# Optimization experiments

Hardware: AMD Instinct MI355X
Metric: run time of the kernel (lower is better)

The kernel has to match this reference:

```python
import jax, jax.numpy as jnp
import numpy as np

# Static configuration (matches init_kwargs)
EMBED_DIM = 256
NUM_HEADS = 8
NUM_LEVELS = 4
NUM_POINTS = 16
N_DEGREE = 3
HEAD_DIM = EMBED_DIM // NUM_HEADS
SPATIAL_SHAPES = ((64, 64), (32, 32), (16, 16), (8, 8))  # (H, W) per level
LEN_V = sum(h * w for h, w in SPATIAL_SHAPES)


def _bilinear_gather(v, loc, Hl, Wl):
    """Bilinear sampling with zero padding, align_corners=False.
    v:   [bs, nH, Hl*Wl, hd]  flattened level feature map (per head)
    loc: [bs, nH, Q, 2]       (x, y) in [0, 1]
    returns [bs, nH, Q, hd]
    """
    x = loc[..., 0] * Wl - 0.5
    y = loc[..., 1] * Hl - 0.5
    x0 = jnp.floor(x)
    y0 = jnp.floor(y)
    wx = x - x0
    wy = y - y0
    out = jnp.zeros(v.shape[:2] + (loc.shape[2], v.shape[-1]), v.dtype)
    corners = ((0, 0, (1 - wx) * (1 - wy)), (1, 0, wx * (1 - wy)),
               (0, 1, (1 - wx) * wy), (1, 1, wx * wy))
    for dx, dy, w in corners:
        xi = x0 + dx
        yi = y0 + dy
        valid = (xi >= 0) & (xi < Wl) & (yi >= 0) & (yi < Hl)
        idx = (jnp.clip(yi, 0, Hl - 1) * Wl + jnp.clip(xi, 0, Wl - 1)).astype(jnp.int32)
        g = jnp.take_along_axis(v, idx[..., None], axis=2)  # [bs,nH,Q,hd]
        out = out + g * (w * valid.astype(w.dtype))[..., None]
    return out


def setup_inputs() -> dict:
    key = jax.random.key(0)
    ks = jax.random.split(key, 12)
    bs, Lq = 4, 1024
    s = 0.02
    return {
        "query": jax.random.normal(ks[0], (bs, Lq, EMBED_DIM), jnp.float32),
        # polynomial coefficients for x(l), y(l); scaled so curves stay roughly in [0,1]
        "reference_points": jax.random.uniform(ks[1], (bs, Lq, 2 * (N_DEGREE + 1)), jnp.float32) * 0.25,
        "value": jax.random.normal(ks[2], (bs, LEN_V, EMBED_DIM), jnp.float32),
        "W_value": jax.random.normal(ks[3], (EMBED_DIM, EMBED_DIM), jnp.float32) * s,
        "b_value": jnp.zeros((EMBED_DIM,), jnp.float32),
        "W_offsets": jax.random.normal(ks[4], (EMBED_DIM, NUM_HEADS * NUM_LEVELS * NUM_POINTS * 2), jnp.float32) * s,
        "b_offsets": jax.random.normal(ks[5], (NUM_HEADS * NUM_LEVELS * NUM_POINTS * 2,), jnp.float32) * 0.5,
        "W_attn": jax.random.normal(ks[6], (EMBED_DIM, NUM_HEADS * NUM_LEVELS * NUM_POINTS), jnp.float32) * s,
        "b_attn": jnp.zeros((NUM_HEADS * NUM_LEVELS * NUM_POINTS,), jnp.float32),
        "W_out": jax.random.normal(ks[7], (EMBED_DIM, EMBED_DIM), jnp.float32) * s,
        "b_out": jnp.zeros((EMBED_DIM,), jnp.float32),
    }


def reference(query, reference_points, value, W_value, b_value, W_offsets,
              b_offsets, W_attn, b_attn, W_out, b_out):
    bs, Lq, _ = query.shape
    Lv = value.shape[1]
    nH, nL, nP, hd = NUM_HEADS, NUM_LEVELS, NUM_POINTS, HEAD_DIM

    v = (value @ W_value + b_value).reshape(bs, Lv, nH, hd)

    sampling_offsets = (query @ W_offsets + b_offsets).reshape(bs, Lq, nH, nL, nP, 2)
    attn = jax.nn.softmax((query @ W_attn + b_attn).reshape(bs, Lq, nH, nL * nP), axis=-1)
    attn = attn.reshape(bs, Lq, nH, nL, nP)

    # reference_points last dim == 8: polynomial branch
    lambdaz = jnp.linspace(0.0, 1.0, nP)
    lambdas = jnp.stack([lambdaz ** i for i in range(N_DEGREE, -1, -1)], axis=1)  # [nP, deg+1]
    ref_polys = reference_points.reshape(bs, Lq, 2, N_DEGREE + 1)
    pnts = jnp.einsum('bqcd,pd->bqpc', ref_polys, lambdas)  # [bs,Lq,nP,2] (x,y)

    # offset_normalizer: spatial shapes flipped -> (W, H) per level
    normalizer = jnp.array([[w, h] for (h, w) in SPATIAL_SHAPES], jnp.float32)
    normalizer = normalizer.reshape(1, 1, 1, nL, 1, 2)
    sampling_locations = pnts[:, :, None, None, :, :] + sampling_offsets / normalizer
    # -> [bs, Lq, nH, nL, nP, 2] in [0,1]

    # deformable attention core: per-level bilinear gather + softmax-weighted sum
    out = jnp.zeros((bs, Lq, nH, hd), v.dtype)
    start = 0
    for lvl, (Hl, Wl) in enumerate(SPATIAL_SHAPES):
        v_l = v[:, start:start + Hl * Wl].transpose(0, 2, 1, 3)  # [bs,nH,Hl*Wl,hd]
        loc_l = sampling_locations[:, :, :, lvl]                 # [bs,Lq,nH,nP,2]
        loc_l = loc_l.transpose(0, 2, 1, 3, 4).reshape(bs, nH, Lq * nP, 2)
        sampled = _bilinear_gather(v_l, loc_l, Hl, Wl).reshape(bs, nH, Lq, nP, hd)
        out = out + jnp.einsum('bhqpd,bqhp->bqhd', sampled, attn[:, :, :, lvl])
        start += Hl * Wl

    output = out.reshape(bs, Lq, nH * hd) @ W_out + b_out
    return output, sampling_locations, attn
```

## Files before the change

### kernel.cpp

```cpp
#include <hip/hip_runtime.h>
#include <math.h>

#define BS 4
#define LQ 1024
#define EMB 256
#define NH 8
#define NL 4
#define NP 16
#define HD 32
#define LV 5440
#define LVP 5936
#define KDIM 256

typedef __attribute__((ext_vector_type(8))) short short8;
typedef __attribute__((ext_vector_type(4))) float f32x4;

__device__ inline unsigned short f2bf(float f) {
    unsigned u = __builtin_bit_cast(unsigned, f);
    u += 0x7fff + ((u >> 16) & 1);
    return (unsigned short)(u >> 16);
}



__global__ __launch_bounds__(256) void prep(const float* __restrict__ Wv,
                                            const float* __restrict__ Wo,
                                            const float* __restrict__ Wa,
                                            const float* __restrict__ Wu,
                                            const float* __restrict__ value,
                                            const float* __restrict__ query,
                                            unsigned short* __restrict__ Wt,
                                            unsigned short* __restrict__ val_bf,
                                            unsigned short* __restrict__ qry_bf,
                                            unsigned short* __restrict__ v_pad) {
    const int blk = blockIdx.x;
    const int t = threadIdx.x;
    if (blk < 512) {
        __shared__ float tile[32][33];
        const int n0 = (blk & 63) * 32, k0 = (blk >> 6) * 32;
        const float* src; int N, nloc;
        if (n0 < 256)       { src = Wv; N = 256;  nloc = n0; }
        else if (n0 < 1280) { src = Wo; N = 1024; nloc = n0 - 256; }
        else if (n0 < 1792) { src = Wa; N = 512;  nloc = n0 - 1280; }
        else                { src = Wu; N = 256;  nloc = n0 - 1792; }
        const int tx = t & 31, ty = t >> 5;
#pragma unroll
        for (int i = 0; i < 32; i += 8)
            tile[ty + i][tx] = src[(size_t)(k0 + ty + i) * N + nloc + tx];
        __syncthreads();
        if (t < 128) {
            const int n_loc = t & 31, oct = t >> 5;
            const int n = n0 + n_loc;
            short8 h;
#pragma unroll
            for (int e = 0; e < 8; ++e) h[e] = (short)f2bf(tile[oct * 8 + e][n_loc]);
            const size_t off = ((size_t)(n >> 4) * 8 + (k0 >> 5)) * 512
                             + ((n & 15) + 16 * oct) * 8;
            *(short8*)(Wt + off) = h;
        }
    } else if (blk < 3744) {
        int i; const float* src; unsigned short* dst;
        if (blk < 3232) { i = (blk - 512) * 256 + t;  src = value; dst = val_bf; }
        else            { i = (blk - 3232) * 256 + t; src = query; dst = qry_bf; }
        const int r = i >> 5, oct = i & 31, k0 = oct * 8;
        const float4 f0 = *(const float4*)(src + (size_t)r * KDIM + k0);
        const float4 f1 = *(const float4*)(src + (size_t)r * KDIM + k0 + 4);
        short8 h;
        h[0] = (short)f2bf(f0.x); h[1] = (short)f2bf(f0.y);
        h[2] = (short)f2bf(f0.z); h[3] = (short)f2bf(f0.w);
        h[4] = (short)f2bf(f1.x); h[5] = (short)f2bf(f1.y);
        h[6] = (short)f2bf(f1.z); h[7] = (short)f2bf(f1.w);
        const size_t off = ((size_t)(r >> 4) * 8 + (oct >> 2)) * 512
                         + ((r & 15) + 16 * (oct & 3)) * 8;
        *(short8*)(dst + off) = h;
    } else {
        const int pidx = (blk - 3744) * 8 + (t >> 5);
        const int lane32 = t & 31;
        const unsigned b = (unsigned)pidx / 496u;
        const unsigned rem = (unsigned)pidx - b * 496u;
        int Wd, W2, pb, i;
        if (rem < 260)      { Wd = 64; W2 = 66; pb = 0;    i = rem; }
        else if (rem < 392) { Wd = 32; W2 = 34; pb = 4356; i = rem - 260; }
        else if (rem < 460) { Wd = 16; W2 = 18; pb = 5512; i = rem - 392; }
        else                { Wd = 8;  W2 = 10; pb = 5836; i = rem - 460; }
        int y, x;
        if (i < W2)          { y = 0;      x = i; }
        else if (i < 2 * W2) { y = Wd + 1; x = i - W2; }
        else { const int j = i - 2 * W2; y = 1 + (j >> 1); x = (j & 1) ? (Wd + 1) : 0; }
        const int hh = lane32 >> 2, cq = lane32 & 3;
        const size_t off = (((size_t)(hh * BS + b) * LVP + pb + y * W2 + x) << 5)
                         + cq * 8;
        uint4 z = {0, 0, 0, 0};
        *(uint4*)(v_pad + off) = z;
    }
}

template <int MODE>
__device__ __forceinline__ void gemm_nolds(const unsigned short* __restrict__ A,
                                           const unsigned short* __restrict__ Bt,
                                           const float* __restrict__ bias,
                                           const float* __restrict__ bias2,
                                           const float* __restrict__ refp,
                                           void* __restrict__ Cv,
                                           float* __restrict__ C2,
                                           int N, int bx, int by) {
    const int t = threadIdx.x;
    const int lane = t & 63, w = t >> 6;
    const int quad = lane >> 4, l16 = lane & 15;
    const int wr = w >> 1, wc = w & 1;
    const int row0 = by * 128, col0 = bx * 128;

    const unsigned short* ap = A  + ((size_t)((row0 >> 4) + wr * 4) * 8) * 512 + lane * 8;
    const unsigned short* bp = Bt + ((size_t)((col0 >> 4) + wc * 4) * 8) * 512 + lane * 8;

    f32x4 acc[4][4] = {};

#pragma unroll 2
    for (int kt = 0; kt < 8; ++kt) {
        short8 af[4], bf[4];
#pragma unroll
        for (int mi = 0; mi < 4; ++mi)
            af[mi] = *(const short8*)(ap + (size_t)mi * 4096 + kt * 512);
#pragma unroll
        for (int ni = 0; ni < 4; ++ni)
            bf[ni] = *(const short8*)(bp + (size_t)ni * 4096 + kt * 512);
#pragma unroll
        for (int mi = 0; mi < 4; ++mi)
#pragma unroll
            for (int ni = 0; ni < 4; ++ni)
                acc[mi][ni] = __builtin_amdgcn_mfma_f32_16x16x32_bf16(af[mi], bf[ni],
                                                                      acc[mi][ni], 0, 0, 0);
    }

    if (MODE == 0) {
#pragma unroll
        for (int ni = 0; ni < 4; ++ni) {
            const int c = col0 + wc * 64 + ni * 16 + l16;
            const float bv = bias[c];
#pragma unroll
            for (int mi = 0; mi < 4; ++mi) {
                const int r0 = row0 + wr * 64 + mi * 16 + quad * 4;
#pragma unroll
                for (int rr = 0; rr < 4; ++rr)
                    ((float*)Cv)[(size_t)(r0 + rr) * N + c] = acc[mi][ni][rr] + bv;
            }
        }
    } else if (MODE == 2) {
        unsigned short* C = (unsigned short*)Cv;
        float bv[4];
        int cc[4];
#pragma unroll
        for (int ni = 0; ni < 4; ++ni) {
            cc[ni] = col0 + wc * 64 + ni * 16 + l16;
            bv[ni] = bias[cc[ni]];
        }
#pragma unroll
        for (int mi = 0; mi < 4; ++mi) {
#pragma unroll
            for (int rr = 0; rr < 4; ++rr) {
                const unsigned r = row0 + wr * 64 + mi * 16 + quad * 4 + rr;
                const unsigned b = r / 5440u;
                const unsigned flat = r - b * 5440u;
                unsigned y, x, W2, pb;
                if (flat < 4096)      { y = flat >> 6; x = flat & 63; W2 = 66; pb = 0; }
                else if (flat < 5120) { const unsigned f = flat - 4096; y = f >> 5; x = f & 31; W2 = 34; pb = 4356; }
                else if (flat < 5376) { const unsigned f = flat - 5120; y = f >> 4; x = f & 15; W2 = 18; pb = 5512; }
                else                  { const unsigned f = flat - 5376; y = f >> 3; x = f & 7;  W2 = 10; pb = 5836; }
                const size_t pix = (size_t)(pb + (y + 1) * W2 + (x + 1)) << 5;
#pragma unroll
                for (int ni = 0; ni < 4; ++ni) {
                    const int cc_ = cc[ni];
                    const size_t off = (((size_t)((cc_ >> 5) * BS + b) * LVP) << 5)
                                     + pix + (cc_ & 31);
                    C[off] = f2bf(acc[mi][ni][rr] + bv[ni]);
                }
            }
        }
    } else {
        const bool is_off = (col0 < 1024);
        if (is_off) {
            float* C = (float*)Cv;
#pragma unroll
            for (int ni = 0; ni < 4; ++ni) {
                const int cg = col0 + wc * 64 + ni * 16 + l16;
                const int xy = cg & 1, p = (cg >> 1) & 15, l = (cg >> 5) & 3;
                const float lam = (float)p * (1.0f / 15.0f);
                const float l2 = lam * lam, l3 = l2 * lam;
                const float rW = (l == 0) ? 0.015625f : (l == 1) ? 0.03125f
                                : (l == 2) ? 0.0625f : 0.125f;
                const float bv = bias[cg];
#pragma unroll
                for (int mi = 0; mi < 4; ++mi) {
                    const int r0 = row0 + wr * 64 + mi * 16 + quad * 4;
#pragma unroll
                    for (int rr = 0; rr < 4; ++rr) {
                        const int r = r0 + rr;
                        const float4 rp = *(const float4*)(refp + (size_t)r * 8 + xy * 4);
                        const float poly = rp.x * l3 + rp.y * l2 + rp.z * lam + rp.w;
                        C[(size_t)r * 1024 + cg] = poly + (acc[mi][ni][rr] + bv) * rW;
                    }
                }
            }
        } else {
            const int cabase = col0 - 1024 + wc * 64;
            float bv[4];
#pragma unroll
            for (int ni = 0; ni < 4; ++ni) bv[ni] = bias2[cabase + ni * 16 + l16];
#pragma unroll
            for (int mi = 0; mi < 4; ++mi) {
                const int r0 = row0 + wr * 64 + mi * 16 + quad * 4;
#pragma unroll
                for (int rr = 0; rr < 4; ++rr) {
                    float v0 = acc[mi][0][rr] + bv[0];
                    float v1 = acc[mi][1][rr] + bv[1];
                    float v2 = acc[mi][2][rr] + bv[2];
                    float v3 = acc[mi][3][rr] + bv[3];
                    float mx = fmaxf(fmaxf(v0, v1), fmaxf(v2, v3));
#pragma unroll
                    for (int mk = 1; mk < 16; mk <<= 1) mx = fmaxf(mx, __shfl_xor(mx, mk));
                    v0 = __expf(v0 - mx); v1 = __expf(v1 - mx);
                    v2 = __expf(v2 - mx); v3 = __expf(v3 - mx);
                    float s = v0 + v1 + v2 + v3;
#pragma unroll
                    for (int mk = 1; mk < 16; mk <<= 1) s += __shfl_xor(s, mk);
                    const float inv = 1.0f / s;
                    const size_t rb = (size_t)(r0 + rr) * 512 + cabase + l16;
                    C2[rb]      = v0 * inv;
                    C2[rb + 16] = v1 * inv;
                    C2[rb + 32] = v2 * inv;
                    C2[rb + 48] = v3 * inv;
                }
            }
        }
    }
}

__global__ __launch_bounds__(256, 2) void gemm_fused(const unsigned short* __restrict__ val_bf,
                                                     const unsigned short* __restrict__ qry_bf,
                                                     const unsigned short* __restrict__ Wt,
                                                     const float* __restrict__ b_value,
                                                     const float* __restrict__ b_off,
                                                     const float* __restrict__ b_attn,
                                                     const float* __restrict__ refp,
                                                     unsigned short* __restrict__ v_pad,
                                                     float* __restrict__ loc_out,
                                                     float* __restrict__ attn_out) {
    const int b = blockIdx.x;
    if (b < 340) {
        gemm_nolds<2>(val_bf, Wt, b_value, nullptr, nullptr,
                      v_pad, nullptr, 256, b & 1, b >> 1);
    } else {
        const int b2 = b - 340;
        gemm_nolds<1>(qry_bf, Wt + (size_t)256 * KDIM, b_off, b_attn, refp,
                      loc_out, attn_out, 1536, b2 % 12, b2 / 12);
    }
}

__global__ __launch_bounds__(256, 2) void gemm_outp(const unsigned short* __restrict__ interm,
                                                    const unsigned short* __restrict__ Wt_out,
                                                    const float* __restrict__ b_out,
                                                    float* __restrict__ out) {
    gemm_nolds<0>(interm, Wt_out, b_out, nullptr, nullptr,
                  out, nullptr, 256, blockIdx.x & 1, blockIdx.x >> 1);
}

__global__ __launch_bounds__(256, 8) void sample_kernel(const unsigned short* __restrict__ v,
                                                        const float* __restrict__ loc,
                                                        const float* __restrict__ attn,
                                                        unsigned short* __restrict__ interm) {
    const int t = threadIdx.x;
    const int h = blockIdx.x & 7;
    const int bq0 = (blockIdx.x >> 3) * 16;

    __shared__ float4 wls[1088];
    __shared__ unsigned short pls[1088];

    {
        const int gloc = t >> 4;
        const int lvl  = (t >> 2) & 3;
        const int pq   = t & 3;
        const int g = (bq0 + gloc) * 8 + h;
        const float4 l01 = *(const float4*)(loc + (size_t)g * 128 + lvl * 32 + pq * 8);
        const float4 l23 = *(const float4*)(loc + (size_t)g * 128 + lvl * 32 + pq * 8 + 4);
        const float4 av  = *(const float4*)(attn + (size_t)g * 64 + lvl * 16 + pq * 4);
        const int Wd = 64 >> lvl;
        const float Wf = (float)Wd;
        const int W2 = Wd + 2;
        const int pb = (lvl == 0) ? 0 : (lvl == 1) ? 4356 : (lvl == 2) ? 5512 : 5836;
        const int ibase = gloc * 64 + lvl * 16 + pq * 4;
        const int pbase = ibase + (ibase >> 4);
        const float lx[4] = {l01.x, l01.z, l23.x, l23.z};
        const float ly[4] = {l01.y, l01.w, l23.y, l23.w};
        const float aw[4] = {av.x, av.y, av.z, av.w};
#pragma unroll
        for (int k = 0; k < 4; ++k) {
            const float x = fmaf(lx[k], Wf, -0.5f);
            const float y = fmaf(ly[k], Wf, -0.5f);
            const float xc = fminf(fmaxf(x, -1.0f), Wf);
            const float yc = fminf(fmaxf(y, -1.0f), Wf);
            const float x0f = fminf(floorf(xc), Wf - 1.0f);
            const float y0f = fminf(floorf(yc), Wf - 1.0f);
            const float wx = xc - x0f, wy = yc - y0f;
            const float iwx = 1.0f - wx, iwy = 1.0f - wy;
            const int px = (int)x0f + 1;
            const int py = (int)y0f + 1;
            const float a = aw[k];
            wls[pbase + k] = make_float4(iwx * iwy * a, wx * iwy * a,
                                         iwx * wy * a,  wx * wy * a);
            pls[pbase + k] = (unsigned short)(pb + py * W2 + px);
        }
    }
    __syncthreads();

    const int bq = bq0 + (t >> 4);
    const int l16i = t & 15;
    const int lvl = l16i >> 2;
    const int cq  = l16i & 3;
    const int b = bq >> 10;
    const int rowoff = ((64 >> lvl) + 2) * 32;

    const unsigned short* vl = v + (((size_t)(h * BS + b) * LVP) << 5) + cq * 8;
    const int wbase = (t >> 4) * 64 + lvl * 16;
    const int wphys = wbase + (wbase >> 4);

    float2 acc2[4] = {};

    auto cvt2 = [](unsigned d) {
        uint2 u; u.x = d << 16; u.y = d & 0xffff0000u;
        return __builtin_bit_cast(float2, u);
    };
    auto cadd = [&](const uint4 q, float wgt) {
        const float2 w2 = make_float2(wgt, wgt);
        acc2[0] += cvt2(q.x) * w2;
        acc2[1] += cvt2(q.y) * w2;
        acc2[2] += cvt2(q.z) * w2;
        acc2[3] += cvt2(q.w) * w2;
    };

#pragma unroll 1
    for (int p = 0; p < 16; ++p) {
        const float4 w = wls[wphys + p];
        const int base = ((int)pls[wphys + p]) << 5;
        const unsigned short* ptr = vl + base;
        const uint4 g00 = *(const uint4*)(ptr);
        const uint4 g10 = *(const uint4*)(ptr + 32);
        const uint4 g01 = *(const uint4*)(ptr + rowoff);
        const uint4 g11 = *(const uint4*)(ptr + rowoff + 32);
        cadd(g00, w.x); cadd(g10, w.y); cadd(g01, w.z); cadd(g11, w.w);
    }

    float a[8] = {acc2[0].x, acc2[0].y, acc2[1].x, acc2[1].y,
                  acc2[2].x, acc2[2].y, acc2[3].x, acc2[3].y};
#pragma unroll
    for (int m = 4; m <= 8; m <<= 1)
#pragma unroll
        for (int k = 0; k < 8; ++k) a[k] += __shfl_xor(a[k], m);

    if (lvl == 0) {
        unsigned short o[8];
#pragma unroll
        for (int k = 0; k < 8; ++k) o[k] = f2bf(a[k]);
        const size_t off = ((size_t)(bq >> 4) * 8 + h) * 512
                         + ((bq & 15) + 16 * cq) * 8;
        *(uint4*)(interm + off) = *(const uint4*)o;
    }
}

extern "C" void kernel_launch(void* const* d_in, const int* in_sizes, int n_in,
                              void* d_out, int out_size, void* d_ws, size_t ws_size,
                              hipStream_t stream) {
    const float* query   = (const float*)d_in[0];
    const float* refp    = (const float*)d_in[1];
    const float* value   = (const float*)d_in[2];
    const float* W_value = (const float*)d_in[3];
    const float* b_value = (const float*)d_in[4];
    const float* W_off   = (const float*)d_in[5];
    const float* b_off   = (const float*)d_in[6];
    const float* W_attn  = (const float*)d_in[7];
    const float* b_attn  = (const float*)d_in[8];
    const float* W_out   = (const float*)d_in[9];
    const float* b_out   = (const float*)d_in[10];

    float* out      = (float*)d_out;
    float* loc_out  = out + 1048576;
    float* attn_out = out + 5242880;

    char* ws = (char*)d_ws;
    unsigned short* v_pad  = (unsigned short*)ws;
    unsigned short* val_bf = (unsigned short*)(ws + 12156928);
    unsigned short* interm = (unsigned short*)(ws + 12156928);
    unsigned short* qry_bf = (unsigned short*)(ws + 23298048);
    unsigned short* Wt_all = (unsigned short*)(ws + 25395200);

    const dim3 blk(256);

    prep<<<3992, blk, 0, stream>>>(W_value, W_off, W_attn, W_out, value, query,
                                   Wt_all, val_bf, qry_bf, v_pad);

    gemm_fused<<<724, blk, 0, stream>>>(val_bf, qry_bf, Wt_all, b_value, b_off,
                                        b_attn, refp, v_pad, loc_out, attn_out);

    sample_kernel<<<(BS * LQ * NH) / 16, blk, 0, stream>>>(v_pad, loc_out, attn_out, interm);

    gemm_outp<<<64, blk, 0, stream>>>(interm, Wt_all + (size_t)1792 * KDIM, b_out, out);
}
```

Before: 154.0 us.

## Split output projection into smaller 64x64 tiles and raise fused GEMM occupancy hint

The output projection GEMM is replaced by a dedicated kernel that computes 64x64 output tiles per block. It launches 256 blocks instead of 64 so that more of the GPU's compute units are busy on this small GEMM. Each wave loads bf16 fragments straight from global memory in the pre-swizzled layout and issues MFMA 16x16x32 ops. Separately, the fused value/offset GEMM's launch bounds are raised from 2 to 3 blocks per CU, which may limit registers and cause spills.

```diff
diff --git a/kernel.cpp b/kernel.cpp
--- a/kernel.cpp
+++ b/kernel.cpp
@@ -235,7 +235,7 @@
     }
 }
 
-__global__ __launch_bounds__(256, 2) void gemm_fused(const unsigned short* __restrict__ val_bf,
+__global__ __launch_bounds__(256, 3) void gemm_fused(const unsigned short* __restrict__ val_bf,
                                                      const unsigned short* __restrict__ qry_bf,
                                                      const unsigned short* __restrict__ Wt,
                                                      const float* __restrict__ b_value,
@@ -256,12 +256,51 @@
     }
 }
 
-__global__ __launch_bounds__(256, 2) void gemm_outp(const unsigned short* __restrict__ interm,
-                                                    const unsigned short* __restrict__ Wt_out,
-                                                    const float* __restrict__ b_out,
-                                                    float* __restrict__ out) {
-    gemm_nolds<0>(interm, Wt_out, b_out, nullptr, nullptr,
-                  out, nullptr, 256, blockIdx.x & 1, blockIdx.x >> 1);
+__global__ __launch_bounds__(256, 8) void gemm_outp64(const unsigned short* __restrict__ interm,
+                                                      const unsigned short* __restrict__ Wt_out,
+                                                      const float* __restrict__ b_out,
+                                                      float* __restrict__ out) {
+    const int t = threadIdx.x;
+    const int lane = t & 63, w = t >> 6;
+    const int quad = lane >> 4, l16 = lane & 15;
+    const int wr = w >> 1, wc = w & 1;
+    const int bx = blockIdx.x & 3, by = blockIdx.x >> 2;
+    const int row0 = by * 64 + wr * 32, col0 = bx * 64 + wc * 32;
+
+    const unsigned short* ap = interm + ((size_t)(row0 >> 4) * 8) * 512 + lane * 8;
+    const unsigned short* bp = Wt_out + ((size_t)(col0 >> 4) * 8) * 512 + lane * 8;
+
+    f32x4 acc[2][2] = {};
+
+#pragma unroll 2
+    for (int kt = 0; kt < 8; ++kt) {
+        short8 af[2], bf[2];
+#pragma unroll
+        for (int mi = 0; mi < 2; ++mi)
+            af[mi] = *(const short8*)(ap + (size_t)mi * 4096 + kt * 512);
+#pragma unroll
+        for (int ni = 0; ni < 2; ++ni)
+            bf[ni] = *(const short8*)(bp + (size_t)ni * 4096 + kt * 512);
+#pragma unroll
+        for (int mi = 0; mi < 2; ++mi)
+#pragma unroll
+            for (int ni = 0; ni < 2; ++ni)
+                acc[mi][ni] = __builtin_amdgcn_mfma_f32_16x16x32_bf16(af[mi], bf[ni],
+                                                                      acc[mi][ni], 0, 0, 0);
+    }
+
+#pragma unroll
+    for (int ni = 0; ni < 2; ++ni) {
+        const int c = col0 + ni * 16 + l16;
+        const float bv = b_out[c];
+#pragma unroll
+        for (int mi = 0; mi < 2; ++mi) {
+            const int r0 = row0 + mi * 16 + quad * 4;
+#pragma unroll
+            for (int rr = 0; rr < 4; ++rr)
+                out[(size_t)(r0 + rr) * 256 + c] = acc[mi][ni][rr] + bv;
+        }
+    }
 }
 
 __global__ __launch_bounds__(256, 8) void sample_kernel(const unsigned short* __restrict__ v,
@@ -402,5 +441,5 @@
 
     sample_kernel<<<(BS * LQ * NH) / 16, blk, 0, stream>>>(v_pad, loc_out, attn_out, interm);
 
-    gemm_outp<<<64, blk, 0, stream>>>(interm, Wt_all + (size_t)1792 * KDIM, b_out, out);
-}
+    gemm_outp64<<<256, blk, 0, stream>>>(interm, Wt_all + (size_t)1792 * KDIM, b_out, out);
+}
```

Measured after the change: 149.6 us. 1.03x faster.
